# Kernel tuning notes

Measured on AMD Instinct MI355X. Metric: run time of the kernel, lower is better.

## Reference

```python
import jax, jax.numpy as jnp
import numpy as np

SEQ_LEN = 4096
EMB = 2048
INP = 457  # totalSyscalls + 1


def setup_inputs() -> dict:
    key = jax.random.key(0)
    ks = jax.random.split(key, 11)
    s_e = 1.0 / np.sqrt(EMB)  # torch LSTM init scale: 1/sqrt(hidden_size)
    s_d = 1.0 / np.sqrt(INP)
    u = lambda k, shape, s: jax.random.uniform(k, shape, jnp.float32, -s, s)
    return {
        "x": jax.random.normal(ks[0], (1, SEQ_LEN, INP), jnp.float32),
        # Encoder LSTM: input_size=INP, hidden_size=EMB
        "enc_Wih": u(ks[1], (4 * EMB, INP), s_e),
        "enc_Whh": u(ks[2], (4 * EMB, EMB), s_e),
        "enc_bih": u(ks[3], (4 * EMB,), s_e),
        "enc_bhh": u(ks[4], (4 * EMB,), s_e),
        # Decoder LSTM: input_size=EMB, hidden_size=INP, proj_size=EMB
        "dec_Wih": u(ks[5], (4 * INP, EMB), s_d),
        "dec_Whh": u(ks[6], (4 * INP, EMB), s_d),
        "dec_bih": u(ks[7], (4 * INP,), s_d),
        "dec_bhh": u(ks[8], (4 * INP,), s_d),
        "dec_Whr": u(ks[9], (EMB, INP), s_d),
    }


def reference(x, enc_Wih, enc_Whh, enc_bih, enc_bhh,
              dec_Wih, dec_Whh, dec_bih, dec_bhh, dec_Whr):
    xs = x.reshape(SEQ_LEN, INP)  # batch dim is structurally 1

    # ---- Encoder: standard LSTM scanned over timesteps (torch gate order i,f,g,o)
    def enc_step(carry, xt):
        h, c = carry
        g = xt @ enc_Wih.T + enc_bih + h @ enc_Whh.T + enc_bhh  # (4*EMB,)
        i, f, gg, o = jnp.split(g, 4)
        c = jax.nn.sigmoid(f) * c + jax.nn.sigmoid(i) * jnp.tanh(gg)
        h = jax.nn.sigmoid(o) * jnp.tanh(c)
        return (h, c), None

    z = jnp.zeros(EMB, x.dtype)
    (h_enc, _), _ = jax.lax.scan(enc_step, (z, z), xs)

    # ---- Decoder: LSTM with projection (hidden_size=INP, proj_size=EMB),
    # feeds its own projected output back in; collects CELL states each step,
    # prepended (torch.cat([cells, out], 0)) => reversed chronological order.
    def dec_step(carry, _):
        xd, h, c = carry
        g = xd @ dec_Wih.T + dec_bih + h @ dec_Whh.T + dec_bhh  # (4*INP,)
        i, f, gg, o = jnp.split(g, 4)
        c = jax.nn.sigmoid(f) * c + jax.nn.sigmoid(i) * jnp.tanh(gg)
        h_raw = jax.nn.sigmoid(o) * jnp.tanh(c)  # (INP,)
        h = h_raw @ dec_Whr.T                     # projected hidden (EMB,)
        return (h, h, c), c

    init = (h_enc, jnp.zeros(EMB, x.dtype), jnp.zeros(INP, x.dtype))
    _, cells = jax.lax.scan(dec_step, init, None, length=SEQ_LEN)  # (SEQ_LEN, INP)
    out = cells[::-1]
    return jax.nn.softmax(out, axis=1)
```

## Files before the change

kernel.cpp:

```cpp
#include <hip/hip_runtime.h>
#include <cmath>

#define SEQ 4096
#define INP 457
#define EMB 2048
#define NWG_E 256
#define NWG_D 16
#define NCPY 8

typedef unsigned long long u64t;
typedef float f32x4 __attribute__((ext_vector_type(4)));
typedef float f32x2 __attribute__((ext_vector_type(2)));

__device__ __forceinline__ float sigf(float v) { return 1.0f / (1.0f + expf(-v)); }

#define PIN(v) asm volatile("" : "+v"(v))

#define QNAN __builtin_bit_cast(float, 0x7fc00000u)

__device__ __forceinline__ f32x4 mall16(const f32x4* p) {
  f32x4 v;
  asm volatile("global_load_dwordx4 %0, %1, off sc0 sc1\n\ts_waitcnt vmcnt(0)"
               : "=v"(v) : "v"(p) : "memory");
  return v;
}
__device__ __forceinline__ f32x2 mall8(const f32x2* p) {
  f32x2 v;
  asm volatile("global_load_dwordx2 %0, %1, off sc0 sc1\n\ts_waitcnt vmcnt(0)"
               : "=v"(v) : "v"(p) : "memory");
  return v;
}

__global__ void bias_kernel(const float* __restrict__ ebih, const float* __restrict__ ebhh,
                            const float* __restrict__ dbih, const float* __restrict__ dbhh,
                            float* __restrict__ bsum, float* __restrict__ btot) {
  int i = blockIdx.x * 256 + threadIdx.x;
  if (i < 4 * EMB) bsum[i] = ebih[i] + ebhh[i];
  if (i < 4 * INP) btot[i] = dbih[i] + dbhh[i];
}

__global__ __launch_bounds__(256) void fold_gemm(const float* __restrict__ dWih,
                                                 const float* __restrict__ dWhh,
                                                 const float* __restrict__ dWhr,
                                                 float* __restrict__ C) {
  const int bx = blockIdx.x, by = blockIdx.y;
  const int tid = threadIdx.x;
  const int tx = tid & 15, ty = tid >> 4;
  __shared__ float As[16][65];
  __shared__ float Bs[16][65];
  float acc[4][4] = {};
  for (int k0 = 0; k0 < EMB; k0 += 16) {
#pragma unroll
    for (int e = 0; e < 4; ++e) {
      int eid = tid * 4 + e;
      int m = eid >> 4, k = eid & 15;
      int row = by * 64 + m;
      float v = 0.0f;
      if (row < 4 * INP) {
        size_t a = (size_t)row * EMB + k0 + k;
        v = dWih[a] + dWhh[a];
      }
      As[k][m] = v;
    }
#pragma unroll
    for (int e = 0; e < 4; ++e) {
      int eid = tid * 4 + e;
      int k = eid >> 6, c = eid & 63;
      int col = bx * 64 + c;
      Bs[k][c] = (col < INP) ? dWhr[(size_t)(k0 + k) * INP + col] : 0.0f;
    }
    __syncthreads();
#pragma unroll
    for (int k = 0; k < 16; ++k) {
      float a0 = As[k][ty * 4 + 0], a1 = As[k][ty * 4 + 1], a2 = As[k][ty * 4 + 2], a3 = As[k][ty * 4 + 3];
      float b0 = Bs[k][tx * 4 + 0], b1 = Bs[k][tx * 4 + 1], b2 = Bs[k][tx * 4 + 2], b3 = Bs[k][tx * 4 + 3];
      acc[0][0] += a0 * b0; acc[0][1] += a0 * b1; acc[0][2] += a0 * b2; acc[0][3] += a0 * b3;
      acc[1][0] += a1 * b0; acc[1][1] += a1 * b1; acc[1][2] += a1 * b2; acc[1][3] += a1 * b3;
      acc[2][0] += a2 * b0; acc[2][1] += a2 * b1; acc[2][2] += a2 * b2; acc[2][3] += a2 * b3;
      acc[3][0] += a3 * b0; acc[3][1] += a3 * b1; acc[3][2] += a3 * b2; acc[3][3] += a3 * b3;
    }
    __syncthreads();
  }
#pragma unroll
  for (int i = 0; i < 4; ++i) {
    int row = by * 64 + ty * 4 + i;
    if (row >= 4 * INP) continue;
#pragma unroll
    for (int j = 0; j < 4; ++j) {
      int col = bx * 64 + tx * 4 + j;
      if (col < 480) C[(size_t)row * 480 + col] = acc[i][j];
    }
  }
}

__global__ __launch_bounds__(512) __attribute__((amdgpu_waves_per_eu(2, 2))) void enc_kernel(
    const float* __restrict__ x, const float* __restrict__ Wih,
    const float* __restrict__ Whh, const float* __restrict__ bsum,
    float* __restrict__ hbuf) {
  const int tid = threadIdx.x;
  const int wg  = blockIdx.x;
  const int j   = tid & 7;
  const int kc  = tid >> 3;
  const int jbase = wg * 8;
  const int mycpy = wg & (NCPY - 1);

  float wh[4][32];
  float wi[4][8];
#pragma unroll
  for (int g = 0; g < 4; ++g) {
    const size_t row = (size_t)(g * EMB + jbase + j);
    const float* wp = Whh + row * EMB + kc * 32;
#pragma unroll
    for (int q = 0; q < 8; ++q) {
      const float4 v = *(const float4*)(wp + 4 * q);
      wh[g][q * 4 + 0] = v.x; wh[g][q * 4 + 1] = v.y;
      wh[g][q * 4 + 2] = v.z; wh[g][q * 4 + 3] = v.w;
    }
    const float* ip = Wih + row * INP;
#pragma unroll
    for (int i = 0; i < 8; ++i) {
      const int c = kc * 8 + i;
      wi[g][i] = (c < INP) ? ip[c] : 0.0f;
    }
  }
#pragma unroll
  for (int g = 0; g < 4; ++g) {
#pragma unroll
    for (int q = 0; q < 32; ++q) PIN(wh[g][q]);
#pragma unroll
    for (int q = 0; q < 8; ++q) PIN(wi[g][q]);
  }

  __shared__ float4 hl4[512];
  __shared__ float4 xl4[128];
  __shared__ float  partbuf[256];
  __shared__ float  b_s[32];
  __shared__ float  c_s[8];
  if (tid < 32) b_s[tid] = bsum[(tid >> 3) * EMB + jbase + (tid & 7)];
  if (tid < 8)  c_s[tid] = 0.0f;
  const int sw = kc & 7;
  const int hphys = tid ^ ((tid >> 3) & 7);
  const int xi = (tid < INP) ? tid : 0;

  for (int t = 0; t < SEQ; ++t) {
    const float xraw = x[(size_t)t * INP + xi];

    const f32x4* gp = (const f32x4*)(hbuf + (size_t)((t & 3) * NCPY + mycpy) * EMB) + tid;
    f32x4 g4;
    for (;;) {
      g4 = mall16(gp);
      if ((g4.x == g4.x) & (g4.y == g4.y) & (g4.z == g4.z) & (g4.w == g4.w)) break;
    }
    hl4[hphys] = make_float4(g4.x, g4.y, g4.z, g4.w);
    ((float*)xl4)[tid] = (tid < INP) ? xraw : 0.0f;

    float4 a0 = make_float4(0, 0, 0, 0), a1 = a0, a2 = a0, a3 = a0;
#pragma unroll
    for (int q = 0; q < 2; ++q) {
      const float4 xq = xl4[kc * 2 + q];
      a0.x += wi[0][q * 4 + 0] * xq.x; a0.y += wi[0][q * 4 + 1] * xq.y; a0.z += wi[0][q * 4 + 2] * xq.z; a0.w += wi[0][q * 4 + 3] * xq.w;
      a1.x += wi[1][q * 4 + 0] * xq.x; a1.y += wi[1][q * 4 + 1] * xq.y; a1.z += wi[1][q * 4 + 2] * xq.z; a1.w += wi[1][q * 4 + 3] * xq.w;
      a2.x += wi[2][q * 4 + 0] * xq.x; a2.y += wi[2][q * 4 + 1] * xq.y; a2.z += wi[2][q * 4 + 2] * xq.z; a2.w += wi[2][q * 4 + 3] * xq.w;
      a3.x += wi[3][q * 4 + 0] * xq.x; a3.y += wi[3][q * 4 + 1] * xq.y; a3.z += wi[3][q * 4 + 2] * xq.z; a3.w += wi[3][q * 4 + 3] * xq.w;
    }
#pragma unroll
    for (int q = 0; q < 8; ++q) {
      const float4 hv = hl4[kc * 8 + (q ^ sw)];
      const int b = q * 4;
      a0.x += wh[0][b + 0] * hv.x; a0.y += wh[0][b + 1] * hv.y; a0.z += wh[0][b + 2] * hv.z; a0.w += wh[0][b + 3] * hv.w;
      a1.x += wh[1][b + 0] * hv.x; a1.y += wh[1][b + 1] * hv.y; a1.z += wh[1][b + 2] * hv.z; a1.w += wh[1][b + 3] * hv.w;
      a2.x += wh[2][b + 0] * hv.x; a2.y += wh[2][b + 1] * hv.y; a2.z += wh[2][b + 2] * hv.z; a2.w += wh[2][b + 3] * hv.w;
      a3.x += wh[3][b + 0] * hv.x; a3.y += wh[3][b + 1] * hv.y; a3.z += wh[3][b + 2] * hv.z; a3.w += wh[3][b + 3] * hv.w;
    }

    float r0 = (a0.x + a0.y) + (a0.z + a0.w);
    float r1 = (a1.x + a1.y) + (a1.z + a1.w);
    float r2 = (a2.x + a2.y) + (a2.z + a2.w);
    float r3 = (a3.x + a3.y) + (a3.z + a3.w);
#pragma unroll
    for (int m = 8; m < 64; m <<= 1) {
      r0 += __shfl_xor(r0, m); r1 += __shfl_xor(r1, m);
      r2 += __shfl_xor(r2, m); r3 += __shfl_xor(r3, m);
    }
    if ((tid & 63) < 8)
      *(float4*)(partbuf + (tid >> 6) * 32 + j * 4) = make_float4(r0, r1, r2, r3);
    __syncthreads();

    if (tid < 8) {
      float* const rearm = hbuf + (size_t)(((t + 3) & 3) * NCPY) * EMB + jbase + tid;
#pragma unroll
      for (int c = 0; c < NCPY; ++c)
        __hip_atomic_store(rearm + (size_t)c * EMB, QNAN,
                           __ATOMIC_RELAXED, __HIP_MEMORY_SCOPE_AGENT);
      float s0 = 0.f, s1 = 0.f, s2 = 0.f, s3 = 0.f;
#pragma unroll
      for (int w = 0; w < 8; ++w) {
        const float4 pv = *(const float4*)(partbuf + w * 32 + tid * 4);
        s0 += pv.x; s1 += pv.y; s2 += pv.z; s3 += pv.w;
      }
      const float gi = s0 + b_s[tid], gf = s1 + b_s[8 + tid];
      const float gg = s2 + b_s[16 + tid], go = s3 + b_s[24 + tid];
      const float cN = sigf(gf) * c_s[tid] + sigf(gi) * tanhf(gg);
      c_s[tid] = cN;
      const float hN = sigf(go) * tanhf(cN);
      asm volatile("s_waitcnt vmcnt(0)" ::: "memory");
      float* const pub = hbuf + (size_t)(((t + 1) & 3) * NCPY) * EMB + jbase + tid;
#pragma unroll
      for (int c = 0; c < NCPY; ++c)
        __hip_atomic_store(pub + (size_t)c * EMB, hN,
                           __ATOMIC_RELAXED, __HIP_MEMORY_SCOPE_AGENT);
    }
  }
}

__global__ __launch_bounds__(512) __attribute__((amdgpu_waves_per_eu(2, 2))) void dec_kernel(
    const float* __restrict__ dWih, const float* __restrict__ Wfold,
    const float* __restrict__ btot, const float* __restrict__ henc,
    float* __restrict__ hraw, float* __restrict__ out) {
  const int tid = threadIdx.x;
  const int wg  = blockIdx.x;
  const int j   = tid & 31;
  const int kc  = tid >> 5;
  const int idx = wg * 32 + j;
  const bool valid = (idx < INP);
  const int id0 = valid ? idx : 0;
  const int l   = tid & 63;
  const int wv  = tid >> 6;
  int gl = l;
  if (gl >= 30) gl -= 30;
  if (gl >= 30) gl -= 30;
  const int gidx = 30 * wv + gl;

  float wd[4][30];
#pragma unroll
  for (int g = 0; g < 4; ++g) {
    const float* wp = Wfold + (size_t)(g * INP + id0) * 480 + kc * 30;
#pragma unroll
    for (int q = 0; q < 15; ++q) {
      const float2 v = valid ? *(const float2*)(wp + 2 * q) : make_float2(0.0f, 0.0f);
      wd[g][q * 2 + 0] = v.x; wd[g][q * 2 + 1] = v.y;
    }
  }
#pragma unroll
  for (int g = 0; g < 4; ++g)
#pragma unroll
    for (int q = 0; q < 30; ++q) PIN(wd[g][q]);

  __shared__ float2 dl2[240];
  __shared__ float  partbuf[1024];
  __shared__ float  b_s[128];
  __shared__ float  c_s[32];
  if (tid < 128) {
    const int ix = wg * 32 + (tid & 31);
    b_s[tid] = (ix < INP) ? btot[(tid >> 5) * INP + ix] : 0.0f;
  }
  if (tid < 32) c_s[tid] = 0.0f;

  for (int t = 0; t < SEQ; ++t) {
    if (t > 0) {
      const f32x2* gp = (const f32x2*)(hraw + (size_t)(t & 3) * 512) + gidx;
      f32x2 g2;
      for (;;) {
        g2 = mall8(gp);
        if ((g2.x == g2.x) & (g2.y == g2.y)) break;
      }
      if (l < 30) dl2[gidx] = make_float2(g2.x, g2.y);
    }

    float2 acc0 = make_float2(0, 0), acc1 = acc0, acc2 = acc0, acc3 = acc0;
    if (t == 0) {
      if (valid) {
#pragma unroll 4
        for (int q = 0; q < 32; ++q) {
          const float4 hv = *(const float4*)(henc + kc * 128 + 4 * q);
          const float4 w0 = *(const float4*)(dWih + (size_t)(0 * INP + idx) * EMB + kc * 128 + 4 * q);
          const float4 w1 = *(const float4*)(dWih + (size_t)(1 * INP + idx) * EMB + kc * 128 + 4 * q);
          const float4 w2 = *(const float4*)(dWih + (size_t)(2 * INP + idx) * EMB + kc * 128 + 4 * q);
          const float4 w3 = *(const float4*)(dWih + (size_t)(3 * INP + idx) * EMB + kc * 128 + 4 * q);
          acc0.x += w0.x * hv.x + w0.z * hv.z; acc0.y += w0.y * hv.y + w0.w * hv.w;
          acc1.x += w1.x * hv.x + w1.z * hv.z; acc1.y += w1.y * hv.y + w1.w * hv.w;
          acc2.x += w2.x * hv.x + w2.z * hv.z; acc2.y += w2.y * hv.y + w2.w * hv.w;
          acc3.x += w3.x * hv.x + w3.z * hv.z; acc3.y += w3.y * hv.y + w3.w * hv.w;
        }
      }
    } else {
#pragma unroll
      for (int q = 0; q < 15; ++q) {
        const float2 hv = dl2[kc * 15 + q];
        acc0.x += wd[0][q * 2] * hv.x; acc0.y += wd[0][q * 2 + 1] * hv.y;
        acc1.x += wd[1][q * 2] * hv.x; acc1.y += wd[1][q * 2 + 1] * hv.y;
        acc2.x += wd[2][q * 2] * hv.x; acc2.y += wd[2][q * 2 + 1] * hv.y;
        acc3.x += wd[3][q * 2] * hv.x; acc3.y += wd[3][q * 2 + 1] * hv.y;
      }
    }
    float r0 = acc0.x + acc0.y, r1 = acc1.x + acc1.y, r2 = acc2.x + acc2.y, r3 = acc3.x + acc3.y;
    r0 += __shfl_xor(r0, 32); r1 += __shfl_xor(r1, 32);
    r2 += __shfl_xor(r2, 32); r3 += __shfl_xor(r3, 32);
    if ((tid & 63) < 32)
      *(float4*)(partbuf + (tid >> 6) * 128 + (tid & 31) * 4) = make_float4(r0, r1, r2, r3);
    __syncthreads();

    if (tid < 32) {
      const int ix = wg * 32 + tid;
      if (ix < 480)
        __hip_atomic_store(hraw + (size_t)((t + 3) & 3) * 512 + ix, QNAN,
                           __ATOMIC_RELAXED, __HIP_MEMORY_SCOPE_AGENT);
      float s0 = 0.f, s1 = 0.f, s2 = 0.f, s3 = 0.f;
#pragma unroll
      for (int w = 0; w < 8; ++w) {
        const float4 pv = *(const float4*)(partbuf + w * 128 + tid * 4);
        s0 += pv.x; s1 += pv.y; s2 += pv.z; s3 += pv.w;
      }
      const float gi = s0 + b_s[tid], gf = s1 + b_s[32 + tid];
      const float gg = s2 + b_s[64 + tid], go = s3 + b_s[96 + tid];
      const float cN = sigf(gf) * c_s[tid] + sigf(gi) * tanhf(gg);
      c_s[tid] = cN;
      const float hrN = sigf(go) * tanhf(cN);
      asm volatile("s_waitcnt vmcnt(0)" ::: "memory");
      if (ix < 480)
        __hip_atomic_store(hraw + (size_t)((t + 1) & 3) * 512 + ix, (ix < INP) ? hrN : 0.0f,
                           __ATOMIC_RELAXED, __HIP_MEMORY_SCOPE_AGENT);
      if (ix < INP) out[(size_t)(SEQ - 1 - t) * INP + ix] = cN;
    }
  }
}

__global__ __launch_bounds__(512) void softmax_kernel(float* __restrict__ out) {
  const int row = blockIdx.x;
  const int tid = threadIdx.x;
  __shared__ float red[512];
  float* rp = out + (size_t)row * INP;
  float v = (tid < INP) ? rp[tid] : -INFINITY;
  red[tid] = v;
  __syncthreads();
#pragma unroll
  for (int off = 256; off > 0; off >>= 1) {
    if (tid < off) red[tid] = fmaxf(red[tid], red[tid + off]);
    __syncthreads();
  }
  const float m = red[0];
  __syncthreads();
  const float e = (tid < INP) ? expf(v - m) : 0.0f;
  red[tid] = e;
  __syncthreads();
#pragma unroll
  for (int off = 256; off > 0; off >>= 1) {
    if (tid < off) red[tid] = red[tid] + red[tid + off];
    __syncthreads();
  }
  const float s = red[0];
  if (tid < INP) rp[tid] = e / s;
}

extern "C" void kernel_launch(void* const* d_in, const int* in_sizes, int n_in,
                              void* d_out, int out_size, void* d_ws, size_t ws_size,
                              hipStream_t stream) {
  const float* x    = (const float*)d_in[0];
  const float* eWih = (const float*)d_in[1];
  const float* eWhh = (const float*)d_in[2];
  const float* ebih = (const float*)d_in[3];
  const float* ebhh = (const float*)d_in[4];
  const float* dWih = (const float*)d_in[5];
  const float* dWhh = (const float*)d_in[6];
  const float* dbih = (const float*)d_in[7];
  const float* dbhh = (const float*)d_in[8];
  const float* dWhr = (const float*)d_in[9];
  float* out = (float*)d_out;
  char* ws = (char*)d_ws;

  float* hbuf  = (float*)(ws + 0);
  float* hraw  = (float*)(ws + 262144);
  float* bsum  = (float*)(ws + 270336);
  float* btot  = (float*)(ws + 303104);
  float* Wfold = (float*)(ws + 311296);

  hipMemsetAsync(ws, 0xFF, 270336, stream);
  hipMemsetAsync(ws, 0x00, 65536, stream);
  bias_kernel<<<40, 256, 0, stream>>>(ebih, ebhh, dbih, dbhh, bsum, btot);
  fold_gemm<<<dim3(8, 29), 256, 0, stream>>>(dWih, dWhh, dWhr, Wfold);
  enc_kernel<<<NWG_E, 512, 0, stream>>>(x, eWih, eWhh, bsum, hbuf);
  dec_kernel<<<NWG_D, 512, 0, stream>>>(dWih, Wfold, btot, hbuf, hraw, out);
  softmax_kernel<<<SEQ, 512, 0, stream>>>(out);
}
```

Measured before the change: 18.65 ms.

## Map each gate row to a wavefront and reduce fully with shuffles

Both recurrent kernels now give each output unit its own wavefront (encoder) or 16-lane group (decoder), so the K-reduction finishes entirely with cross-lane shuffles. This removes the shared-memory partial-sum buffer and the single-thread gate epilogue. Bias and cell state are kept in registers, and publish and re-arm stores are spread across lanes. In exchange, a barrier is added after the shared-memory staging of h, the LDS bank swizzle is dropped, and the gate math is computed redundantly across lanes.

```diff
diff --git a/kernel.cpp b/kernel.cpp
--- a/kernel.cpp
+++ b/kernel.cpp
@@ -15,7 +15,6 @@
 __device__ __forceinline__ float sigf(float v) { return 1.0f / (1.0f + expf(-v)); }
 
 #define PIN(v) asm volatile("" : "+v"(v))
-
 #define QNAN __builtin_bit_cast(float, 0x7fc00000u)
 
 __device__ __forceinline__ f32x4 mall16(const f32x4* p) {
@@ -99,8 +98,8 @@
     float* __restrict__ hbuf) {
   const int tid = threadIdx.x;
   const int wg  = blockIdx.x;
-  const int j   = tid & 7;
-  const int kc  = tid >> 3;
+  const int w   = tid >> 6;
+  const int l   = tid & 63;
   const int jbase = wg * 8;
   const int mycpy = wg & (NCPY - 1);
 
@@ -108,8 +107,8 @@
   float wi[4][8];
 #pragma unroll
   for (int g = 0; g < 4; ++g) {
-    const size_t row = (size_t)(g * EMB + jbase + j);
-    const float* wp = Whh + row * EMB + kc * 32;
+    const size_t row = (size_t)(g * EMB + jbase + w);
+    const float* wp = Whh + row * EMB + l * 32;
 #pragma unroll
     for (int q = 0; q < 8; ++q) {
       const float4 v = *(const float4*)(wp + 4 * q);
@@ -119,7 +118,7 @@
     const float* ip = Wih + row * INP;
 #pragma unroll
     for (int i = 0; i < 8; ++i) {
-      const int c = kc * 8 + i;
+      const int c = l * 8 + i;
       wi[g][i] = (c < INP) ? ip[c] : 0.0f;
     }
   }
@@ -130,16 +129,14 @@
 #pragma unroll
     for (int q = 0; q < 8; ++q) PIN(wi[g][q]);
   }
+  const float bg0 = bsum[0 * EMB + jbase + w];
+  const float bg1 = bsum[1 * EMB + jbase + w];
+  const float bg2 = bsum[2 * EMB + jbase + w];
+  const float bg3 = bsum[3 * EMB + jbase + w];
+  float c_reg = 0.0f;
 
   __shared__ float4 hl4[512];
   __shared__ float4 xl4[128];
-  __shared__ float  partbuf[256];
-  __shared__ float  b_s[32];
-  __shared__ float  c_s[8];
-  if (tid < 32) b_s[tid] = bsum[(tid >> 3) * EMB + jbase + (tid & 7)];
-  if (tid < 8)  c_s[tid] = 0.0f;
-  const int sw = kc & 7;
-  const int hphys = tid ^ ((tid >> 3) & 7);
   const int xi = (tid < INP) ? tid : 0;
 
   for (int t = 0; t < SEQ; ++t) {
@@ -151,13 +148,14 @@
       g4 = mall16(gp);
       if ((g4.x == g4.x) & (g4.y == g4.y) & (g4.z == g4.z) & (g4.w == g4.w)) break;
     }
-    hl4[hphys] = make_float4(g4.x, g4.y, g4.z, g4.w);
+    hl4[tid] = make_float4(g4.x, g4.y, g4.z, g4.w);
     ((float*)xl4)[tid] = (tid < INP) ? xraw : 0.0f;
+    __syncthreads();
 
     float4 a0 = make_float4(0, 0, 0, 0), a1 = a0, a2 = a0, a3 = a0;
 #pragma unroll
     for (int q = 0; q < 2; ++q) {
-      const float4 xq = xl4[kc * 2 + q];
+      const float4 xq = xl4[l * 2 + q];
       a0.x += wi[0][q * 4 + 0] * xq.x; a0.y += wi[0][q * 4 + 1] * xq.y; a0.z += wi[0][q * 4 + 2] * xq.z; a0.w += wi[0][q * 4 + 3] * xq.w;
       a1.x += wi[1][q * 4 + 0] * xq.x; a1.y += wi[1][q * 4 + 1] * xq.y; a1.z += wi[1][q * 4 + 2] * xq.z; a1.w += wi[1][q * 4 + 3] * xq.w;
       a2.x += wi[2][q * 4 + 0] * xq.x; a2.y += wi[2][q * 4 + 1] * xq.y; a2.z += wi[2][q * 4 + 2] * xq.z; a2.w += wi[2][q * 4 + 3] * xq.w;
@@ -165,7 +163,7 @@
     }
 #pragma unroll
     for (int q = 0; q < 8; ++q) {
-      const float4 hv = hl4[kc * 8 + (q ^ sw)];
+      const float4 hv = hl4[l * 8 + q];
       const int b = q * 4;
       a0.x += wh[0][b + 0] * hv.x; a0.y += wh[0][b + 1] * hv.y; a0.z += wh[0][b + 2] * hv.z; a0.w += wh[0][b + 3] * hv.w;
       a1.x += wh[1][b + 0] * hv.x; a1.y += wh[1][b + 1] * hv.y; a1.z += wh[1][b + 2] * hv.z; a1.w += wh[1][b + 3] * hv.w;
@@ -178,37 +176,22 @@
     float r2 = (a2.x + a2.y) + (a2.z + a2.w);
     float r3 = (a3.x + a3.y) + (a3.z + a3.w);
 #pragma unroll
-    for (int m = 8; m < 64; m <<= 1) {
+    for (int m = 1; m < 64; m <<= 1) {
       r0 += __shfl_xor(r0, m); r1 += __shfl_xor(r1, m);
       r2 += __shfl_xor(r2, m); r3 += __shfl_xor(r3, m);
     }
-    if ((tid & 63) < 8)
-      *(float4*)(partbuf + (tid >> 6) * 32 + j * 4) = make_float4(r0, r1, r2, r3);
-    __syncthreads();
-
-    if (tid < 8) {
-      float* const rearm = hbuf + (size_t)(((t + 3) & 3) * NCPY) * EMB + jbase + tid;
-#pragma unroll
-      for (int c = 0; c < NCPY; ++c)
-        __hip_atomic_store(rearm + (size_t)c * EMB, QNAN,
-                           __ATOMIC_RELAXED, __HIP_MEMORY_SCOPE_AGENT);
-      float s0 = 0.f, s1 = 0.f, s2 = 0.f, s3 = 0.f;
-#pragma unroll
-      for (int w = 0; w < 8; ++w) {
-        const float4 pv = *(const float4*)(partbuf + w * 32 + tid * 4);
-        s0 += pv.x; s1 += pv.y; s2 += pv.z; s3 += pv.w;
-      }
-      const float gi = s0 + b_s[tid], gf = s1 + b_s[8 + tid];
-      const float gg = s2 + b_s[16 + tid], go = s3 + b_s[24 + tid];
-      const float cN = sigf(gf) * c_s[tid] + sigf(gi) * tanhf(gg);
-      c_s[tid] = cN;
-      const float hN = sigf(go) * tanhf(cN);
-      asm volatile("s_waitcnt vmcnt(0)" ::: "memory");
-      float* const pub = hbuf + (size_t)(((t + 1) & 3) * NCPY) * EMB + jbase + tid;
-#pragma unroll
-      for (int c = 0; c < NCPY; ++c)
-        __hip_atomic_store(pub + (size_t)c * EMB, hN,
-                           __ATOMIC_RELAXED, __HIP_MEMORY_SCOPE_AGENT);
+
+    const float gi = r0 + bg0, gf = r1 + bg1, gg = r2 + bg2, go = r3 + bg3;
+    const float cN = sigf(gf) * c_reg + sigf(gi) * tanhf(gg);
+    c_reg = cN;
+    const float hN = sigf(go) * tanhf(cN);
+    asm volatile("s_waitcnt vmcnt(0)" ::: "memory");
+    if (l < 8) {
+      __hip_atomic_store(hbuf + (size_t)(((t + 1) & 3) * NCPY + l) * EMB + jbase + w, hN,
+                         __ATOMIC_RELAXED, __HIP_MEMORY_SCOPE_AGENT);
+    } else if (l < 16) {
+      __hip_atomic_store(hbuf + (size_t)(((t + 3) & 3) * NCPY + (l - 8)) * EMB + jbase + w, QNAN,
+                         __ATOMIC_RELAXED, __HIP_MEMORY_SCOPE_AGENT);
     }
   }
 }
@@ -219,22 +202,18 @@
     float* __restrict__ hraw, float* __restrict__ out) {
   const int tid = threadIdx.x;
   const int wg  = blockIdx.x;
-  const int j   = tid & 31;
-  const int kc  = tid >> 5;
-  const int idx = wg * 32 + j;
+  const int w   = tid >> 6;
+  const int l   = tid & 63;
+  const int kk  = l & 15;
+  const int jl  = w * 4 + (l >> 4);
+  const int idx = wg * 32 + jl;
   const bool valid = (idx < INP);
   const int id0 = valid ? idx : 0;
-  const int l   = tid & 63;
-  const int wv  = tid >> 6;
-  int gl = l;
-  if (gl >= 30) gl -= 30;
-  if (gl >= 30) gl -= 30;
-  const int gidx = 30 * wv + gl;
 
   float wd[4][30];
 #pragma unroll
   for (int g = 0; g < 4; ++g) {
-    const float* wp = Wfold + (size_t)(g * INP + id0) * 480 + kc * 30;
+    const float* wp = Wfold + (size_t)(g * INP + id0) * 480 + kk * 30;
 #pragma unroll
     for (int q = 0; q < 15; ++q) {
       const float2 v = valid ? *(const float2*)(wp + 2 * q) : make_float2(0.0f, 0.0f);
@@ -246,25 +225,26 @@
 #pragma unroll
     for (int q = 0; q < 30; ++q) PIN(wd[g][q]);
 
+  const float bg0 = valid ? btot[0 * INP + idx] : 0.0f;
+  const float bg1 = valid ? btot[1 * INP + idx] : 0.0f;
+  const float bg2 = valid ? btot[2 * INP + idx] : 0.0f;
+  const float bg3 = valid ? btot[3 * INP + idx] : 0.0f;
+  float c_reg = 0.0f;
+
   __shared__ float2 dl2[240];
-  __shared__ float  partbuf[1024];
-  __shared__ float  b_s[128];
-  __shared__ float  c_s[32];
-  if (tid < 128) {
-    const int ix = wg * 32 + (tid & 31);
-    b_s[tid] = (ix < INP) ? btot[(tid >> 5) * INP + ix] : 0.0f;
-  }
-  if (tid < 32) c_s[tid] = 0.0f;
 
   for (int t = 0; t < SEQ; ++t) {
     if (t > 0) {
-      const f32x2* gp = (const f32x2*)(hraw + (size_t)(t & 3) * 512) + gidx;
-      f32x2 g2;
-      for (;;) {
-        g2 = mall8(gp);
-        if ((g2.x == g2.x) & (g2.y == g2.y)) break;
+      if (tid < 240) {
+        const f32x2* gp = (const f32x2*)(hraw + (size_t)(t & 3) * 512) + tid;
+        f32x2 g2;
+        for (;;) {
+          g2 = mall8(gp);
+          if ((g2.x == g2.x) & (g2.y == g2.y)) break;
+        }
+        dl2[tid] = make_float2(g2.x, g2.y);
       }
-      if (l < 30) dl2[gidx] = make_float2(g2.x, g2.y);
+      __syncthreads();
     }
 
     float2 acc0 = make_float2(0, 0), acc1 = acc0, acc2 = acc0, acc3 = acc0;
@@ -272,11 +252,11 @@
       if (valid) {
 #pragma unroll 4
         for (int q = 0; q < 32; ++q) {
-          const float4 hv = *(const float4*)(henc + kc * 128 + 4 * q);
-          const float4 w0 = *(const float4*)(dWih + (size_t)(0 * INP + idx) * EMB + kc * 128 + 4 * q);
-          const float4 w1 = *(const float4*)(dWih + (size_t)(1 * INP + idx) * EMB + kc * 128 + 4 * q);
-          const float4 w2 = *(const float4*)(dWih + (size_t)(2 * INP + idx) * EMB + kc * 128 + 4 * q);
-          const float4 w3 = *(const float4*)(dWih + (size_t)(3 * INP + idx) * EMB + kc * 128 + 4 * q);
+          const float4 hv = *(const float4*)(henc + kk * 128 + 4 * q);
+          const float4 w0 = *(const float4*)(dWih + (size_t)(0 * INP + idx) * EMB + kk * 128 + 4 * q);
+          const float4 w1 = *(const float4*)(dWih + (size_t)(1 * INP + idx) * EMB + kk * 128 + 4 * q);
+          const float4 w2 = *(const float4*)(dWih + (size_t)(2 * INP + idx) * EMB + kk * 128 + 4 * q);
+          const float4 w3 = *(const float4*)(dWih + (size_t)(3 * INP + idx) * EMB + kk * 128 + 4 * q);
           acc0.x += w0.x * hv.x + w0.z * hv.z; acc0.y += w0.y * hv.y + w0.w * hv.w;
           acc1.x += w1.x * hv.x + w1.z * hv.z; acc1.y += w1.y * hv.y + w1.w * hv.w;
           acc2.x += w2.x * hv.x + w2.z * hv.z; acc2.y += w2.y * hv.y + w2.w * hv.w;
@@ -286,7 +266,7 @@
     } else {
 #pragma unroll
       for (int q = 0; q < 15; ++q) {
-        const float2 hv = dl2[kc * 15 + q];
+        const float2 hv = dl2[kk * 15 + q];
         acc0.x += wd[0][q * 2] * hv.x; acc0.y += wd[0][q * 2 + 1] * hv.y;
         acc1.x += wd[1][q * 2] * hv.x; acc1.y += wd[1][q * 2 + 1] * hv.y;
         acc2.x += wd[2][q * 2] * hv.x; acc2.y += wd[2][q * 2 + 1] * hv.y;
@@ -294,33 +274,26 @@
       }
     }
     float r0 = acc0.x + acc0.y, r1 = acc1.x + acc1.y, r2 = acc2.x + acc2.y, r3 = acc3.x + acc3.y;
-    r0 += __shfl_xor(r0, 32); r1 += __shfl_xor(r1, 32);
-    r2 += __shfl_xor(r2, 32); r3 += __shfl_xor(r3, 32);
-    if ((tid & 63) < 32)
-      *(float4*)(partbuf + (tid >> 6) * 128 + (tid & 31) * 4) = make_float4(r0, r1, r2, r3);
-    __syncthreads();
-
-    if (tid < 32) {
-      const int ix = wg * 32 + tid;
-      if (ix < 480)
-        __hip_atomic_store(hraw + (size_t)((t + 3) & 3) * 512 + ix, QNAN,
+#pragma unroll
+    for (int m = 1; m < 16; m <<= 1) {
+      r0 += __shfl_xor(r0, m); r1 += __shfl_xor(r1, m);
+      r2 += __shfl_xor(r2, m); r3 += __shfl_xor(r3, m);
+    }
+
+    const float gi = r0 + bg0, gf = r1 + bg1, gg = r2 + bg2, go = r3 + bg3;
+    const float cN = sigf(gf) * c_reg + sigf(gi) * tanhf(gg);
+    c_reg = cN;
+    const float hrN = sigf(go) * tanhf(cN);
+    asm volatile("s_waitcnt vmcnt(0)" ::: "memory");
+    if (kk == 0) {
+      if (idx < 480)
+        __hip_atomic_store(hraw + (size_t)((t + 1) & 3) * 512 + idx, valid ? hrN : 0.0f,
                            __ATOMIC_RELAXED, __HIP_MEMORY_SCOPE_AGENT);
-      float s0 = 0.f, s1 = 0.f, s2 = 0.f, s3 = 0.f;
-#pragma unroll
-      for (int w = 0; w < 8; ++w) {
-        const float4 pv = *(const float4*)(partbuf + w * 128 + tid * 4);
-        s0 += pv.x; s1 += pv.y; s2 += pv.z; s3 += pv.w;
-      }
-      const float gi = s0 + b_s[tid], gf = s1 + b_s[32 + tid];
-      const float gg = s2 + b_s[64 + tid], go = s3 + b_s[96 + tid];
-      const float cN = sigf(gf) * c_s[tid] + sigf(gi) * tanhf(gg);
-      c_s[tid] = cN;
-      const float hrN = sigf(go) * tanhf(cN);
-      asm volatile("s_waitcnt vmcnt(0)" ::: "memory");
-      if (ix < 480)
-        __hip_atomic_store(hraw + (size_t)((t + 1) & 3) * 512 + ix, (ix < INP) ? hrN : 0.0f,
+      if (valid) out[(size_t)(SEQ - 1 - t) * INP + idx] = cN;
+    } else if (kk == 1) {
+      if (idx < 480)
+        __hip_atomic_store(hraw + (size_t)((t + 3) & 3) * 512 + idx, QNAN,
                            __ATOMIC_RELAXED, __HIP_MEMORY_SCOPE_AGENT);
-      if (ix < INP) out[(size_t)(SEQ - 1 - t) * INP + ix] = cN;
     }
   }
 }
```

After: 57.86 ms. +210.3%, slower.
